# Optimization experiments

Hardware: AMD Instinct MI355X
Metric: run time of the kernel (lower is better)

Reference implementation:

```python
import jax, jax.numpy as jnp
import numpy as np

EPS = 1e-3  # Keras BatchNormalization default epsilon
PARTITIONS = 4


def setup_inputs() -> dict:
    key = jax.random.key(0)
    k1, k2 = jax.random.split(key)
    B, H, W, C = 256, 32, 32, 256
    x = jax.random.normal(k1, (B, H, W, C), dtype=jnp.float32)
    gamma = jnp.ones((PARTITIONS, C), dtype=jnp.float32)
    beta = jnp.zeros((PARTITIONS, C), dtype=jnp.float32)
    perm = jax.random.permutation(k2, B).astype(jnp.int32)
    return {"x": x, "gamma": gamma, "beta": beta, "perm": perm}


def reference(x, gamma, beta, perm):
    B, H, W, C = x.shape
    P = PARTITIONS
    ps = B // P  # partition size (B divisible by P)
    # shuffle gather along batch
    shuffled = x[perm]                               # [B,H,W,C]
    parts = shuffled.reshape(P, ps, H, W, C)         # [P,ps,H,W,C]
    # per-partition, per-channel batch statistics (training-mode BN, biased var)
    mean = jnp.mean(parts, axis=(1, 2, 3), keepdims=True)  # [P,1,1,1,C]
    var = jnp.var(parts, axis=(1, 2, 3), keepdims=True)    # [P,1,1,1,C]
    g = gamma[:, None, None, None, :]
    b = beta[:, None, None, None, :]
    normalized = (parts - mean) * jax.lax.rsqrt(var + EPS) * g + b
    shuffled_normalized = normalized.reshape(B, H, W, C)
    # inverse gather (un-shuffle)
    inv_perm = jnp.argsort(perm)
    return shuffled_normalized[inv_perm]
```

## Files before the change

### kernel.cpp

```cpp
#include <hip/hip_runtime.h>

#define EPS 0.001f
#define HW_POS 1024
#define NCH 256
#define NCG 64
#define NB 256
#define NP 4
#define PS 64
#define SPLIT 4
#define POS_PER_BLOCK (HW_POS / SPLIT)
#define N_PER_PC 65536.0f

__global__ __launch_bounds__(256) void k_partial(const float4* __restrict__ x,
                                                 float4* __restrict__ psum,
                                                 float4* __restrict__ psq) {
    const int slot  = blockIdx.x;
    const int b     = slot >> 2;
    const int chunk = slot & (SPLIT - 1);
    const int t     = threadIdx.x;
    const int cg    = t & 63;
    const int srow  = t >> 6;

    const float4* xb = x + (size_t)b * (HW_POS * NCG);
    const int s0 = chunk * POS_PER_BLOCK;

    float4 s = make_float4(0.f, 0.f, 0.f, 0.f);
    float4 q = make_float4(0.f, 0.f, 0.f, 0.f);
    #pragma unroll 4
    for (int si = s0 + srow; si < s0 + POS_PER_BLOCK; si += 4) {
        float4 v = xb[(size_t)si * NCG + cg];
        s.x += v.x; s.y += v.y; s.z += v.z; s.w += v.w;
        q.x += v.x * v.x; q.y += v.y * v.y; q.z += v.z * v.z; q.w += v.w * v.w;
    }

    __shared__ float4 ls[4][64];
    __shared__ float4 lq[4][64];
    ls[srow][cg] = s;
    lq[srow][cg] = q;
    __syncthreads();

    if (srow == 0) {
        float4 a0 = ls[0][cg], a1 = ls[1][cg], a2 = ls[2][cg], a3 = ls[3][cg];
        float4 b0 = lq[0][cg], b1 = lq[1][cg], b2 = lq[2][cg], b3 = lq[3][cg];
        float4 ts = make_float4(a0.x + a1.x + a2.x + a3.x,
                                a0.y + a1.y + a2.y + a3.y,
                                a0.z + a1.z + a2.z + a3.z,
                                a0.w + a1.w + a2.w + a3.w);
        float4 tq = make_float4(b0.x + b1.x + b2.x + b3.x,
                                b0.y + b1.y + b2.y + b3.y,
                                b0.z + b1.z + b2.z + b3.z,
                                b0.w + b1.w + b2.w + b3.w);
        psum[(size_t)slot * NCG + cg] = ts;
        psq [(size_t)slot * NCG + cg] = tq;
    }
}

__global__ __launch_bounds__(256) void k_finalize(const float* __restrict__ psum,
                                                  const float* __restrict__ psq,
                                                  const float* __restrict__ gamma,
                                                  const float* __restrict__ beta,
                                                  const int* __restrict__ perm,
                                                  float* __restrict__ scale,
                                                  float* __restrict__ shift) {
    const int p = blockIdx.x;
    const int c = threadIdx.x;

    float s = 0.f, q = 0.f;
    for (int j = 0; j < PS; ++j) {
        const int b = perm[p * PS + j];
        #pragma unroll
        for (int k = 0; k < SPLIT; ++k) {
            const int slot = b * SPLIT + k;
            s += psum[(size_t)slot * NCH + c];
            q += psq [(size_t)slot * NCH + c];
        }
    }
    const float mean = s * (1.0f / N_PER_PC);
    const float var  = q * (1.0f / N_PER_PC) - mean * mean;
    const float inv  = rsqrtf(var + EPS);
    const float g    = gamma[p * NCH + c];
    const float sc   = g * inv;
    scale[p * NCH + c] = sc;
    shift[p * NCH + c] = beta[p * NCH + c] - mean * sc;
}

__global__ __launch_bounds__(256) void k_norm(const float4* __restrict__ x,
                                              const float4* __restrict__ scale4,
                                              const float4* __restrict__ shift4,
                                              const int* __restrict__ perm,
                                              float4* __restrict__ out) {
    const int blk   = blockIdx.x;
    const int j     = blk >> 2;
    const int chunk = blk & (SPLIT - 1);
    const int b     = perm[j];
    const int p     = j >> 6;
    const int t     = threadIdx.x;
    const int cg    = t & 63;
    const int srow  = t >> 6;

    const float4 sc = scale4[p * NCG + cg];
    const float4 sh = shift4[p * NCG + cg];

    const float4* xb = x   + (size_t)b * (HW_POS * NCG);
    float4*       ob = (float4*)out + (size_t)b * (HW_POS * NCG);
    const int s0 = chunk * POS_PER_BLOCK;

    #pragma unroll 4
    for (int si = s0 + srow; si < s0 + POS_PER_BLOCK; si += 4) {
        float4 v = xb[(size_t)si * NCG + cg];
        v.x = v.x * sc.x + sh.x;
        v.y = v.y * sc.y + sh.y;
        v.z = v.z * sc.z + sh.z;
        v.w = v.w * sc.w + sh.w;
        ob[(size_t)si * NCG + cg] = v;
    }
}

extern "C" void kernel_launch(void* const* d_in, const int* in_sizes, int n_in,
                              void* d_out, int out_size, void* d_ws, size_t ws_size,
                              hipStream_t stream) {
    const float* x     = (const float*)d_in[0];
    const float* gamma = (const float*)d_in[1];
    const float* beta  = (const float*)d_in[2];
    const int*   perm  = (const int*)d_in[3];
    float* out = (float*)d_out;

    char* ws = (char*)d_ws;
    float* psum  = (float*)(ws);
    float* psq   = (float*)(ws + (size_t)NB * SPLIT * NCH * sizeof(float));
    float* scale = (float*)(ws + 2 * (size_t)NB * SPLIT * NCH * sizeof(float));
    float* shift = scale + NP * NCH;

    k_partial<<<NB * SPLIT, 256, 0, stream>>>((const float4*)x,
                                              (float4*)psum, (float4*)psq);
    k_finalize<<<NP, NCH, 0, stream>>>(psum, psq, gamma, beta, perm, scale, shift);
    k_norm<<<NB * SPLIT, 256, 0, stream>>>((const float4*)x,
                                           (const float4*)scale, (const float4*)shift,
                                           perm, (float4*)out);
}
```

Baseline: 511.2 us.

## Accumulate partition stats via atomics and fold finalize into normalize kernel

Partial-sum blocks now look up their partition through perm and atomically add per-channel sums and squares into a small per-partition accumulator, zeroed by a tiny kernel. The separate finalize kernel is removed, and each normalize block computes scale and shift itself from the accumulators. The normalize kernel walks blocks in reverse order so its first reads hit data the stats pass touched last and may still be in cache, and both loops unroll by 8. This trades the finalize launch and the partial-buffer traffic for atomic contention on 2048 addresses and repeated per-block rsqrt work.

```diff
diff --git a/kernel.cpp b/kernel.cpp
--- a/kernel.cpp
+++ b/kernel.cpp
@@ -11,12 +11,21 @@
 #define POS_PER_BLOCK (HW_POS / SPLIT)
 #define N_PER_PC 65536.0f
 
+__global__ __launch_bounds__(256) void k_zero(float* __restrict__ acc) {
+    const int i = threadIdx.x;
+    #pragma unroll
+    for (int k = 0; k < 8; ++k) acc[k * 256 + i] = 0.f;
+}
+
 __global__ __launch_bounds__(256) void k_partial(const float4* __restrict__ x,
-                                                 float4* __restrict__ psum,
-                                                 float4* __restrict__ psq) {
+                                                 const int* __restrict__ perm,
+                                                 float* __restrict__ asum,
+                                                 float* __restrict__ asq) {
     const int slot  = blockIdx.x;
-    const int b     = slot >> 2;
+    const int j     = slot >> 2;
     const int chunk = slot & (SPLIT - 1);
+    const int b     = perm[j];
+    const int p     = j >> 6;
     const int t     = threadIdx.x;
     const int cg    = t & 63;
     const int srow  = t >> 6;
@@ -26,7 +35,7 @@
 
     float4 s = make_float4(0.f, 0.f, 0.f, 0.f);
     float4 q = make_float4(0.f, 0.f, 0.f, 0.f);
-    #pragma unroll 4
+    #pragma unroll 8
     for (int si = s0 + srow; si < s0 + POS_PER_BLOCK; si += 4) {
         float4 v = xb[(size_t)si * NCG + cg];
         s.x += v.x; s.y += v.y; s.z += v.z; s.w += v.w;
@@ -42,54 +51,32 @@
     if (srow == 0) {
         float4 a0 = ls[0][cg], a1 = ls[1][cg], a2 = ls[2][cg], a3 = ls[3][cg];
         float4 b0 = lq[0][cg], b1 = lq[1][cg], b2 = lq[2][cg], b3 = lq[3][cg];
-        float4 ts = make_float4(a0.x + a1.x + a2.x + a3.x,
-                                a0.y + a1.y + a2.y + a3.y,
-                                a0.z + a1.z + a2.z + a3.z,
-                                a0.w + a1.w + a2.w + a3.w);
-        float4 tq = make_float4(b0.x + b1.x + b2.x + b3.x,
-                                b0.y + b1.y + b2.y + b3.y,
-                                b0.z + b1.z + b2.z + b3.z,
-                                b0.w + b1.w + b2.w + b3.w);
-        psum[(size_t)slot * NCG + cg] = ts;
-        psq [(size_t)slot * NCG + cg] = tq;
+        float ts[4] = { a0.x + a1.x + a2.x + a3.x,
+                        a0.y + a1.y + a2.y + a3.y,
+                        a0.z + a1.z + a2.z + a3.z,
+                        a0.w + a1.w + a2.w + a3.w };
+        float tq[4] = { b0.x + b1.x + b2.x + b3.x,
+                        b0.y + b1.y + b2.y + b3.y,
+                        b0.z + b1.z + b2.z + b3.z,
+                        b0.w + b1.w + b2.w + b3.w };
+        float* sp = asum + p * NCH + cg * 4;
+        float* qp = asq  + p * NCH + cg * 4;
+        #pragma unroll
+        for (int k = 0; k < 4; ++k) {
+            atomicAdd(sp + k, ts[k]);
+            atomicAdd(qp + k, tq[k]);
+        }
     }
 }
 
-__global__ __launch_bounds__(256) void k_finalize(const float* __restrict__ psum,
-                                                  const float* __restrict__ psq,
-                                                  const float* __restrict__ gamma,
-                                                  const float* __restrict__ beta,
-                                                  const int* __restrict__ perm,
-                                                  float* __restrict__ scale,
-                                                  float* __restrict__ shift) {
-    const int p = blockIdx.x;
-    const int c = threadIdx.x;
-
-    float s = 0.f, q = 0.f;
-    for (int j = 0; j < PS; ++j) {
-        const int b = perm[p * PS + j];
-        #pragma unroll
-        for (int k = 0; k < SPLIT; ++k) {
-            const int slot = b * SPLIT + k;
-            s += psum[(size_t)slot * NCH + c];
-            q += psq [(size_t)slot * NCH + c];
-        }
-    }
-    const float mean = s * (1.0f / N_PER_PC);
-    const float var  = q * (1.0f / N_PER_PC) - mean * mean;
-    const float inv  = rsqrtf(var + EPS);
-    const float g    = gamma[p * NCH + c];
-    const float sc   = g * inv;
-    scale[p * NCH + c] = sc;
-    shift[p * NCH + c] = beta[p * NCH + c] - mean * sc;
-}
-
 __global__ __launch_bounds__(256) void k_norm(const float4* __restrict__ x,
-                                              const float4* __restrict__ scale4,
-                                              const float4* __restrict__ shift4,
+                                              const float* __restrict__ asum,
+                                              const float* __restrict__ asq,
+                                              const float* __restrict__ gamma,
+                                              const float* __restrict__ beta,
                                               const int* __restrict__ perm,
                                               float4* __restrict__ out) {
-    const int blk   = blockIdx.x;
+    const int blk   = (int)gridDim.x - 1 - (int)blockIdx.x;
     const int j     = blk >> 2;
     const int chunk = blk & (SPLIT - 1);
     const int b     = perm[j];
@@ -98,14 +85,30 @@
     const int cg    = t & 63;
     const int srow  = t >> 6;
 
-    const float4 sc = scale4[p * NCG + cg];
-    const float4 sh = shift4[p * NCG + cg];
+    float4 sc, sh;
+    {
+        float scv[4], shv[4];
+        #pragma unroll
+        for (int k = 0; k < 4; ++k) {
+            const int c   = cg * 4 + k;
+            const float s = asum[p * NCH + c];
+            const float q = asq [p * NCH + c];
+            const float mean = s * (1.0f / N_PER_PC);
+            const float var  = q * (1.0f / N_PER_PC) - mean * mean;
+            const float inv  = rsqrtf(var + EPS);
+            const float g    = gamma[p * NCH + c];
+            scv[k] = g * inv;
+            shv[k] = beta[p * NCH + c] - mean * scv[k];
+        }
+        sc = make_float4(scv[0], scv[1], scv[2], scv[3]);
+        sh = make_float4(shv[0], shv[1], shv[2], shv[3]);
+    }
 
     const float4* xb = x   + (size_t)b * (HW_POS * NCG);
-    float4*       ob = (float4*)out + (size_t)b * (HW_POS * NCG);
+    float4*       ob = out + (size_t)b * (HW_POS * NCG);
     const int s0 = chunk * POS_PER_BLOCK;
 
-    #pragma unroll 4
+    #pragma unroll 8
     for (int si = s0 + srow; si < s0 + POS_PER_BLOCK; si += 4) {
         float4 v = xb[(size_t)si * NCG + cg];
         v.x = v.x * sc.x + sh.x;
@@ -125,16 +128,11 @@
     const int*   perm  = (const int*)d_in[3];
     float* out = (float*)d_out;
 
-    char* ws = (char*)d_ws;
-    float* psum  = (float*)(ws);
-    float* psq   = (float*)(ws + (size_t)NB * SPLIT * NCH * sizeof(float));
-    float* scale = (float*)(ws + 2 * (size_t)NB * SPLIT * NCH * sizeof(float));
-    float* shift = scale + NP * NCH;
+    float* asum = (float*)d_ws;
+    float* asq  = asum + NP * NCH;
 
-    k_partial<<<NB * SPLIT, 256, 0, stream>>>((const float4*)x,
-                                              (float4*)psum, (float4*)psq);
-    k_finalize<<<NP, NCH, 0, stream>>>(psum, psq, gamma, beta, perm, scale, shift);
-    k_norm<<<NB * SPLIT, 256, 0, stream>>>((const float4*)x,
-                                           (const float4*)scale, (const float4*)shift,
-                                           perm, (float4*)out);
+    k_zero<<<1, 256, 0, stream>>>(asum);
+    k_partial<<<NB * SPLIT, 256, 0, stream>>>((const float4*)x, perm, asum, asq);
+    k_norm<<<NB * SPLIT, 256, 0, stream>>>((const float4*)x, asum, asq,
+                                           gamma, beta, perm, (float4*)out);
 }
```

Result: no change. 507.2 us (-0.8%).
